# Kernel tuning notes

Hardware: AMD Instinct MI355X
Metric: run time of the kernel (lower is better)

The kernel has to match this reference:

```python
import jax, jax.numpy as jnp
import numpy as np
from jax import lax

K = 8            # number of object slots
H = 250          # hidden / fc_size
EPS = 1e-5
DN = ('NCHW', 'OIHW', 'NCHW')


def ln_all(x):
    # F.layer_norm over all non-batch dims, no affine params (torch init: w=1,b=0)
    ax = tuple(range(1, x.ndim))
    m = jnp.mean(x, ax, keepdims=True)
    v = jnp.var(x, ax, keepdims=True)
    return (x - m) * lax.rsqrt(v + EPS)


def ln_last(x):
    # nn.LayerNorm(feat) -> last dim only
    m = jnp.mean(x, -1, keepdims=True)
    v = jnp.var(x, -1, keepdims=True)
    return (x - m) * lax.rsqrt(v + EPS)


def conv(x, w, b):
    # torch Conv2d(k=4, s=2, p=1), NCHW
    y = lax.conv_general_dilated(x, w, (2, 2), [(1, 1), (1, 1)], dimension_numbers=DN)
    return y + b[None, :, None, None]


def up4(x):
    return jnp.repeat(jnp.repeat(x, 4, axis=2), 4, axis=3)


def setup_inputs():
    ks = jax.random.split(jax.random.key(0), 20)
    bk = 48 * K
    p = lambda i, shape, s: jax.random.normal(ks[i], shape, jnp.float32) * s
    z = lambda n: jnp.zeros((n,), jnp.float32)
    return dict(
        x=p(0, (bk, 4096), 1.0),
        state=p(1, (bk, H), 1.0),
        # encoder convs (OIHW) + fc
        c1w=p(2, (16, 1, 4, 4), 0.25), c1b=z(16),
        c2w=p(3, (32, 16, 4, 4), 0.06), c2b=z(32),
        c3w=p(4, (64, 32, 4, 4), 0.04), c3b=z(64),
        efc_w=p(5, (4096, 512), 0.016), efc_b=z(512),
        # R_NEM (weights stored as [in, out])
        renc_w=p(6, (H, H), 0.06), renc_b=z(H),
        core_w=p(7, (2 * H, H), 0.045), core_b=z(H),
        ctx_w=p(8, (H, H), 0.06), ctx_b=z(H),
        att1_w=p(9, (H, 100), 0.06), att1_b=z(100),
        att2_w=p(10, (100, 1), 0.1), att2_b=z(1),
        out_w=p(11, (2 * H + 512, H), 0.03), out_b=z(H),
        # decoder fcs + convs
        dfc1_w=p(12, (H, 512), 0.06), dfc1_b=z(512),
        dfc2_w=p(13, (512, 4096), 0.045), dfc2_b=z(4096),
        d1w=p(14, (32, 64, 4, 4), 0.03), d1b=z(32),
        d2w=p(15, (16, 32, 4, 4), 0.045), d2b=z(16),
        d3w=p(16, (1, 16, 4, 4), 0.06), d3b=z(1),
    )


def reference(x, state, c1w, c1b, c2w, c2b, c3w, c3b, efc_w, efc_b,
              renc_w, renc_b, core_w, core_b, ctx_w, ctx_b,
              att1_w, att1_b, att2_w, att2_b, out_w, out_b,
              dfc1_w, dfc1_b, dfc2_w, dfc2_b, d1w, d1b, d2w, d2b, d3w, d3b):
    bk = x.shape[0]
    b = bk // K

    # ---------------- EncoderLayer ----------------
    def inwrap(h, w, bias):  # InputWrapper conv branch: NHWC -> permute(0,3,2,1) -> conv -> back
        y = conv(jnp.transpose(h, (0, 3, 2, 1)), w, bias)
        return jax.nn.elu(ln_all(jnp.transpose(y, (0, 3, 2, 1))))

    h = x.reshape(bk, 64, 64, 1)
    h = inwrap(h, c1w, c1b)                 # (bk,32,32,16)
    h = inwrap(h, c2w, c2b)                 # (bk,16,16,32)
    h = inwrap(h, c3w, c3b)                 # (bk,8,8,64)
    h = h.reshape(bk, -1)                   # (bk,4096)
    h = jax.nn.elu(ln_last(h @ efc_w + efc_b))   # (bk,512)

    # ---------------- R_NEM (RecurrentLayer) ----------------
    s1 = jax.nn.relu(ln_last(state @ renc_w + renc_b))   # (bk,H)
    s1r = s1.reshape(b, K, H)
    idx = np.array([[j for j in range(K) if j != i] for i in range(K)])  # (K,K-1)
    cs = s1r[:, idx, :]                                    # context: (b,K,K-1,H)
    fs = jnp.broadcast_to(s1r[:, :, None, :], cs.shape)    # focus copies
    pair = jnp.concatenate([fs, cs], axis=-1)              # (b,K,K-1,2H)
    core = jax.nn.relu(ln_last(pair @ core_w + core_b))    # (b,K,K-1,H)
    ctx = jax.nn.relu(ln_last(core @ ctx_w + ctx_b))       # (b,K,K-1,H)
    att = jax.nn.sigmoid(jnp.tanh(ln_last(core @ att1_w + att1_b)) @ att2_w + att2_b)  # (b,K,K-1,1)
    effect = jnp.sum(ctx * att, axis=2).reshape(bk, H)     # attention-weighted sum over K-1
    total = jnp.concatenate([s1, effect, h], axis=1)       # (bk, 2H+512)
    new_state = total @ out_w + out_b                      # (bk,H)
    xr = jax.nn.sigmoid(ln_last(new_state))
    state_out = jax.nn.sigmoid(new_state)

    # ---------------- DecoderLayer ----------------
    d = jax.nn.relu(ln_last(xr @ dfc1_w + dfc1_b))         # (bk,512)
    d = jax.nn.relu(ln_last(d @ dfc2_w + dfc2_b))          # (bk,4096)
    d = d.reshape(bk, 8, 8, 64)

    def outwrap(t, w, bias):
        y = conv(up4(jnp.transpose(t, (0, 3, 2, 1))), w, bias)
        return jnp.transpose(y, (0, 3, 2, 1))

    d = jax.nn.relu(ln_all(outwrap(d, d1w, d1b)))          # (bk,16,16,32)
    d = jax.nn.relu(ln_all(outwrap(d, d2w, d2b)))          # (bk,32,32,16)
    d = jax.nn.sigmoid(outwrap(d, d3w, d3b))               # (bk,64,64,1), no LN
    x_out = d.reshape(bk, -1)                              # (bk,4096)
    return x_out, state_out
```

## Files before the change

### kernel.cpp

```cpp
#include <hip/hip_runtime.h>
#include <hip/hip_bf16.h>
#include <math.h>

typedef __attribute__((ext_vector_type(8))) short bf16x8;
typedef __attribute__((ext_vector_type(4))) float f32x4;

__device__ __forceinline__ float eluf(float v){ return v > 0.f ? v : expm1f(v); }
__device__ __forceinline__ float sigf(float v){ return 1.f/(1.f+expf(-v)); }
__device__ __forceinline__ unsigned short f2bf(float f){
  unsigned u = __float_as_uint(f);
  u += 0x7FFFu + ((u >> 16) & 1u);
  return (unsigned short)(u >> 16);
}
__device__ __forceinline__ float bf2f(short s){
  return __uint_as_float(((unsigned)(unsigned short)s) << 16);
}

__device__ __forceinline__ void block_reduce2(float& a, float& b, float* sbuf){
  __syncthreads();
  for (int off = 32; off; off >>= 1){
    a += __shfl_down(a, off);
    b += __shfl_down(b, off);
  }
  int lane = threadIdx.x & 63, w = threadIdx.x >> 6;
  if (lane == 0){ sbuf[2*w] = a; sbuf[2*w+1] = b; }
  __syncthreads();
  if (threadIdx.x == 0){
    int nw = blockDim.x >> 6;
    float sa = 0.f, sb = 0.f;
    for (int i = 0; i < nw; i++){ sa += sbuf[2*i]; sb += sbuf[2*i+1]; }
    sbuf[0] = sa; sbuf[1] = sb;
  }
  __syncthreads();
  a = sbuf[0]; b = sbuf[1];
}

__device__ __forceinline__ float fold_sum(const float* __restrict__ w, int O, int I,
                                          int o, int i, int pa, int pb, int da, int db){
  float s = 0.f;
  for (int kh = 0; kh < 4; kh++){
    bool inh = (pb==0) ? (db==0 ? (kh==0) : (kh>=1)) : (db==0 ? (kh<=2) : (kh==3));
    if (!inh) continue;
    for (int kw = 0; kw < 4; kw++){
      bool inw = (pa==0) ? (da==0 ? (kw==0) : (kw>=1)) : (da==0 ? (kw<=2) : (kw==3));
      if (!inw) continue;
      s += w[((o*I + i)*4 + kh)*4 + kw];
    }
  }
  return s;
}
__device__ __forceinline__ void fold_elem(const float* __restrict__ w, float* __restrict__ CW,
                                          int O, int I, int l){
  int o = l % O; int q = l / O;
  int da = q & 1, db = (q>>1)&1, pa = (q>>2)&1, pb = (q>>3)&1, i = q>>4;
  CW[(((pb*2+pa)*4 + db*2+da)*I + i)*O + o] = fold_sum(w, O, I, o, i, pa, pb, da, db);
}
__device__ __forceinline__ void cvtc2_elem(const float* __restrict__ w, short* __restrict__ D, int l){
  int i = l & 15, t = (l>>4) & 15, o = l>>8;
  D[l] = (short)f2bf(w[(o*16 + i)*16 + t]);
}
__device__ __forceinline__ void cvtc3_elem(const float* __restrict__ w, short* __restrict__ D, int l){
  int i = l & 31, t = (l>>5) & 15, o = l>>9;
  D[l] = (short)f2bf(w[(o*32 + i)*16 + t]);
}
__device__ __forceinline__ void foldd1_elem(const float* __restrict__ w, short* __restrict__ D, int l){
  int i = l & 63, tap = (l>>6)&3, o = (l>>8)&31, ph = l>>13;
  D[l] = (short)f2bf(fold_sum(w, 32, 64, o, i, ph&1, ph>>1, tap&1, tap>>1));
}
__device__ __forceinline__ void foldd2_elem(const float* __restrict__ w, short* __restrict__ D, int l){
  int i = l & 31, tap = (l>>5)&3, o = (l>>7)&15, ph = l>>11;
  D[l] = (short)f2bf(fold_sum(w, 16, 32, o, i, ph&1, ph>>1, tap&1, tap>>1));
}

__global__ __launch_bounds__(256) void prep_combined(
  const float* __restrict__ efc,  short* __restrict__ Defc,
  const float* __restrict__ dfc2, short* __restrict__ Ddfc2,
  const float* __restrict__ outw, short* __restrict__ Dout,
  const float* __restrict__ corew,short* __restrict__ Dcore,
  const float* __restrict__ dfc1, short* __restrict__ Ddfc1,
  const float* __restrict__ renc, short* __restrict__ Drenc,
  const float* __restrict__ ctx,  short* __restrict__ Dctx,
  const float* __restrict__ att1, short* __restrict__ Datt1,
  const float* __restrict__ d3w, float* __restrict__ CWT3,
  const float* __restrict__ c2w, short* __restrict__ BtC2,
  const float* __restrict__ c3w, short* __restrict__ BtC3,
  const float* __restrict__ d1w, short* __restrict__ BD1,
  const float* __restrict__ d2w, short* __restrict__ BD2,
  const float* __restrict__ state, short* __restrict__ SBF,
  short* __restrict__ TOTb)
{
  int bx = blockIdx.x;
  if (bx >= 1192){
    const int F3=256, P2=F3+8192, P3=P2+32768, P4=P3+32768, P5=P4+8192,
              ST=P5+98304, TOTAL=ST+4608;
    for (int l = (bx-1192)*256 + threadIdx.x; l < TOTAL; l += 256*256){
      if (l < F3)      fold_elem(d3w, CWT3, 1, 16, l);
      else if (l < P2) cvtc2_elem(c2w, BtC2, l - F3);
      else if (l < P3) cvtc3_elem(c3w, BtC3, l - P2);
      else if (l < P4) foldd1_elem(d1w, BD1, l - P3);
      else if (l < P5) foldd2_elem(d2w, BD2, l - P4);
      else if (l < ST){
        int q = l - P5;
        int n = q >> 8, k = q & 255;
        SBF[q] = (k < 250) ? (short)f2bf(state[n*250 + k]) : (short)0;
      } else {
        int q = l - ST;
        int row = q / 12, cc = q % 12;
        int col = cc < 6 ? 250 + cc : 506 + (cc - 6);
        TOTb[row*1024 + col] = 0;
      }
    }
    return;
  }
  const float* W; short* D; int K, N, Kp, base, mode = 0;
  if      (bx < 512) { W=efc;  D=Defc;  K=4096; N=512;  Kp=4096; base=0;    }
  else if (bx < 1024){ W=dfc2; D=Ddfc2; K=512;  N=4096; Kp=512;  base=512;  }
  else if (bx < 1088){ W=outw; D=Dout;  K=1012; N=250;  Kp=1024; base=1024; mode=2; }
  else if (bx < 1120){ W=corew;D=Dcore; K=500;  N=250;  Kp=512;  base=1088; mode=1; }
  else if (bx < 1152){ W=dfc1; D=Ddfc1; K=250;  N=512;  Kp=256;  base=1120; }
  else if (bx < 1168){ W=renc; D=Drenc; K=250;  N=250;  Kp=256;  base=1152; }
  else if (bx < 1184){ W=ctx;  D=Dctx;  K=250;  N=250;  Kp=256;  base=1168; }
  else               { W=att1; D=Datt1; K=250;  N=100;  Kp=256;  base=1184; }
  int t = bx - base;
  int tpr = Kp >> 6;
  int tk = t % tpr, tn = t / tpr;
  __shared__ short tile[64][65];
  int c = threadIdx.x & 63, r4 = threadIdx.x >> 6;
  int n0 = tn*64, k0 = tk*64;
  #pragma unroll 4
  for (int p = 0; p < 16; p++){
    int r = r4*16 + p;
    int k = k0 + r, n = n0 + c;
    int ksrc = k; bool valid;
    if (mode == 0) valid = (k < K);
    else if (mode == 1){ valid = (k < 250) || (k >= 256 && k < 506); ksrc = k < 256 ? k : k - 6; }
    else { valid = (k < 250) || (k >= 256 && k < 506) || (k >= 512);
           ksrc = k < 256 ? k : (k < 512 ? k - 6 : k - 12); }
    float v = (valid && n < N) ? W[(size_t)ksrc*N + n] : 0.f;
    tile[c][r] = (short)f2bf(v);
  }
  __syncthreads();
  #pragma unroll 4
  for (int p = 0; p < 16; p++){
    int nn = r4*16 + p;
    int n = n0 + nn;
    if (n < N) D[(size_t)n*Kp + k0 + c] = tile[nn][c];
  }
}

__global__ __launch_bounds__(256) void gemm_mfma(
    const short* __restrict__ Ab, const short* __restrict__ Bt,
    float* __restrict__ P, int M, int N, int Kp, int Kc)
{
  __shared__ __align__(16) short As[64*32];
  __shared__ __align__(16) short Bs[64*32];
  int tid = threadIdx.x;
  int bm = blockIdx.y*64, bn = blockIdx.x*64;
  int kb = blockIdx.z * Kc;
  int kend = kb + Kc;

  int r = tid >> 2, c = tid & 3;
  const short* Arow = Ab + (size_t)(bm + r)*Kp;
  int gn = bn + r;
  bool bval = gn < N;
  const short* Brow = Bt + (size_t)gn*Kp;

  uint4 hA, hB;
  auto load_regs = [&](int k0){
    hA = *(const uint4*)&Arow[k0 + c*8];
    hB = bval ? *(const uint4*)&Brow[k0 + c*8] : make_uint4(0,0,0,0);
  };
  auto write_lds = [&](){
    *(uint4*)&As[r*32 + c*8] = hA;
    *(uint4*)&Bs[r*32 + c*8] = hB;
  };

  int wave = tid >> 6;
  int ln = tid & 15, quad = (tid >> 4) & 3;
  int wr = (wave >> 1) * 32, wc = (wave & 1) * 32;

  f32x4 zero = {0.f, 0.f, 0.f, 0.f};
  f32x4 acc[2][2] = {{zero, zero}, {zero, zero}};

  load_regs(kb);
  write_lds();
  __syncthreads();
  for (int k0 = kb; k0 < kend; k0 += 32){
    int nxt = k0 + 32;
    if (nxt < kend) load_regs(nxt);
    bf16x8 a0 = *(const bf16x8*)&As[(wr +      ln)*32 + quad*8];
    bf16x8 a1 = *(const bf16x8*)&As[(wr + 16 + ln)*32 + quad*8];
    bf16x8 b0 = *(const bf16x8*)&Bs[(wc +      ln)*32 + quad*8];
    bf16x8 b1 = *(const bf16x8*)&Bs[(wc + 16 + ln)*32 + quad*8];
    acc[0][0] = __builtin_amdgcn_mfma_f32_16x16x32_bf16(a0, b0, acc[0][0], 0, 0, 0);
    acc[0][1] = __builtin_amdgcn_mfma_f32_16x16x32_bf16(a0, b1, acc[0][1], 0, 0, 0);
    acc[1][0] = __builtin_amdgcn_mfma_f32_16x16x32_bf16(a1, b0, acc[1][0], 0, 0, 0);
    acc[1][1] = __builtin_amdgcn_mfma_f32_16x16x32_bf16(a1, b1, acc[1][1], 0, 0, 0);
    __syncthreads();
    if (nxt < kend){ write_lds(); __syncthreads(); }
  }

  float* Pout = P + (size_t)blockIdx.z*M*N;
  #pragma unroll
  for (int t = 0; t < 2; t++)
    #pragma unroll
    for (int u = 0; u < 2; u++)
      #pragma unroll
      for (int j = 0; j < 4; j++){
        int row = bm + wr + t*16 + quad*4 + j;
        int col = bn + wc + u*16 + ln;
        if (col < N) Pout[(size_t)row*N + col] = acc[t][u][j];
      }
}

__global__ __launch_bounds__(256) void gemm_core_mfma(
    const short* __restrict__ Tb, const short* __restrict__ Bt,
    float* __restrict__ P, int M, int N, int Kc)
{
  __shared__ __align__(16) short As[64*32];
  __shared__ __align__(16) short Bs[64*32];
  int tid = threadIdx.x;
  int bm = blockIdx.y*64, bn = blockIdx.x*64;
  int kb = blockIdx.z * Kc;
  int kend = kb + Kc;

  int r = tid >> 2, c = tid & 3;
  int gr = bm + r;
  int jj2 = gr % 7, fi2 = gr / 7;
  int ii = fi2 & 7, j2 = fi2 >> 3;
  int jidx = jj2 < ii ? jj2 : jj2 + 1;
  const short* own = Tb + (size_t)fi2*1024;
  const short* oth = Tb + (size_t)(j2*8 + jidx)*1024;
  int gn = bn + r;
  bool bval = gn < N;
  const short* Brow = Bt + (size_t)gn*512;

  uint4 hA, hB;
  auto load_regs = [&](int k0){
    int kk = k0 + c*8;
    const short* src = (kk & 256) ? oth : own;
    hA = *(const uint4*)&src[kk & 255];
    hB = bval ? *(const uint4*)&Brow[kk] : make_uint4(0,0,0,0);
  };
  auto write_lds = [&](){
    *(uint4*)&As[r*32 + c*8] = hA;
    *(uint4*)&Bs[r*32 + c*8] = hB;
  };

  int wave = tid >> 6;
  int ln = tid & 15, quad = (tid >> 4) & 3;
  int wr = (wave >> 1) * 32, wc = (wave & 1) * 32;

  f32x4 zero = {0.f, 0.f, 0.f, 0.f};
  f32x4 acc[2][2] = {{zero, zero}, {zero, zero}};

  load_regs(kb);
  write_lds();
  __syncthreads();
  for (int k0 = kb; k0 < kend; k0 += 32){
    int nxt = k0 + 32;
    if (nxt < kend) load_regs(nxt);
    bf16x8 a0 = *(const bf16x8*)&As[(wr +      ln)*32 + quad*8];
    bf16x8 a1 = *(const bf16x8*)&As[(wr + 16 + ln)*32 + quad*8];
    bf16x8 b0 = *(const bf16x8*)&Bs[(wc +      ln)*32 + quad*8];
    bf16x8 b1 = *(const bf16x8*)&Bs[(wc + 16 + ln)*32 + quad*8];
    acc[0][0] = __builtin_amdgcn_mfma_f32_16x16x32_bf16(a0, b0, acc[0][0], 0, 0, 0);
    acc[0][1] = __builtin_amdgcn_mfma_f32_16x16x32_bf16(a0, b1, acc[0][1], 0, 0, 0);
    acc[1][0] = __builtin_amdgcn_mfma_f32_16x16x32_bf16(a1, b0, acc[1][0], 0, 0, 0);
    acc[1][1] = __builtin_amdgcn_mfma_f32_16x16x32_bf16(a1, b1, acc[1][1], 0, 0, 0);
    __syncthreads();
    if (nxt < kend){ write_lds(); __syncthreads(); }
  }

  float* Pout = P + (size_t)blockIdx.z*M*N;
  #pragma unroll
  for (int t = 0; t < 2; t++)
    #pragma unroll
    for (int u = 0; u < 2; u++)
      #pragma unroll
      for (int j = 0; j < 4; j++){
        int row = bm + wr + t*16 + quad*4 + j;
        int col = bn + wc + u*16 + ln;
        if (col < N) Pout[(size_t)row*N + col] = acc[t][u][j];
      }
}

__global__ __launch_bounds__(256) void reduce_ln(
    const float* __restrict__ Pp, const float* __restrict__ bias,
    void* __restrict__ outp, int M, int N, int KS, int os, int act, int obf)
{
  __shared__ float rowbuf[4096];
  __shared__ float sbuf[16];
  int row = blockIdx.x;
  size_t MN = (size_t)M*N;
  float s = 0.f, s2 = 0.f;
  for (int c = threadIdx.x; c < N; c += 256){
    float v = bias[c];
    for (int ks = 0; ks < KS; ks++) v += Pp[ks*MN + (size_t)row*N + c];
    rowbuf[c] = v; s += v; s2 += v*v;
  }
  block_reduce2(s, s2, sbuf);
  float m = s / N;
  float r = rsqrtf(s2/N - m*m + 1e-5f);
  for (int c = threadIdx.x; c < N; c += 256){
    float v = (rowbuf[c]-m)*r;
    if (act == 1) v = fmaxf(v, 0.f);
    else if (act == 2) v = eluf(v);
    else if (act == 3) v = tanhf(v);
    if (obf) ((short*)outp)[(size_t)row*os + c] = f2bf(v);
    else     ((float*)outp)[(size_t)row*os + c] = v;
  }
}

__global__ __launch_bounds__(256) void reduce_ns(
    const float* __restrict__ Pp, const float* __restrict__ bias,
    short* __restrict__ XRb, float* __restrict__ so, int M, int N, int KS)
{
  __shared__ float rowbuf[256];
  __shared__ float sbuf[16];
  int row = blockIdx.x;
  size_t MN = (size_t)M*N;
  float s = 0.f, s2 = 0.f;
  for (int c = threadIdx.x; c < N; c += 256){
    float v = bias[c];
    for (int ks = 0; ks < KS; ks++) v += Pp[ks*MN + (size_t)row*N + c];
    rowbuf[c] = v; s += v; s2 += v*v;
  }
  block_reduce2(s, s2, sbuf);
  float m = s / N;
  float r = rsqrtf(s2/N - m*m + 1e-5f);
  for (int c = threadIdx.x; c < N; c += 256){
    float v = rowbuf[c];
    XRb[(size_t)row*256 + c] = f2bf(sigf((v-m)*r));
    so[(size_t)row*N + c] = sigf(v);
  }
}

__global__ __launch_bounds__(448) void ctx_att_effect(
    const float* __restrict__ Pc, const float* __restrict__ ctx_b,
    const float* __restrict__ Pa, const float* __restrict__ att1_b,
    const float* __restrict__ w2, const float* __restrict__ b2,
    short* __restrict__ tot)
{
  __shared__ float ctxs[7][250];
  __shared__ float att_s[7];
  int fi = blockIdx.x, tid = threadIdx.x;
  int jj = tid >> 6, lane = tid & 63;
  const size_t MN = (size_t)2688*250, MN2 = (size_t)2688*100;
  int row = fi*7 + jj;
  float vv[4];
  float s = 0.f, s2 = 0.f;
  #pragma unroll
  for (int t = 0; t < 4; t++){
    int c = lane + t*64;
    float v = 0.f;
    if (c < 250) v = ctx_b[c] + Pc[(size_t)row*250 + c] + Pc[MN + (size_t)row*250 + c];
    vv[t] = v; s += v; s2 += v*v;
  }
  #pragma unroll
  for (int off = 32; off; off >>= 1){ s += __shfl_down(s, off); s2 += __shfl_down(s2, off); }
  s = __shfl(s, 0); s2 = __shfl(s2, 0);
  float m = s*(1.f/250.f);
  float r = rsqrtf(s2*(1.f/250.f) - m*m + 1e-5f);
  #pragma unroll
  for (int t = 0; t < 4; t++){
    int c = lane + t*64;
    if (c < 250) ctxs[jj][c] = fmaxf((vv[t]-m)*r, 0.f);
  }
  float va[2];
  s = 0.f; s2 = 0.f;
  #pragma unroll
  for (int t = 0; t < 2; t++){
    int c = lane + t*64;
    float v = 0.f;
    if (c < 100){
      v = att1_b[c];
      #pragma unroll
      for (int ks = 0; ks < 4; ks++) v += Pa[ks*MN2 + (size_t)row*100 + c];
    }
    va[t] = v; s += v; s2 += v*v;
  }
  #pragma unroll
  for (int off = 32; off; off >>= 1){ s += __shfl_down(s, off); s2 += __shfl_down(s2, off); }
  s = __shfl(s, 0); s2 = __shfl(s2, 0);
  m = s*0.01f;
  r = rsqrtf(s2*0.01f - m*m + 1e-5f);
  float d = 0.f;
  #pragma unroll
  for (int t = 0; t < 2; t++){
    int c = lane + t*64;
    if (c < 100) d += tanhf((va[t]-m)*r)*w2[c];
  }
  #pragma unroll
  for (int off = 32; off; off >>= 1) d += __shfl_down(d, off);
  if (lane == 0) att_s[jj] = sigf(d + b2[0]);
  __syncthreads();
  for (int h = tid; h < 250; h += 448){
    float sum = 0.f;
    #pragma unroll
    for (int q = 0; q < 7; q++) sum += ctxs[q][h]*att_s[q];
    tot[(size_t)fi*1024 + 256 + h] = f2bf(sum);
  }
}

__global__ __launch_bounds__(256) void enc_conv1_ig(
    const float* __restrict__ x, const float* __restrict__ w, const float* __restrict__ bias,
    short* __restrict__ outp)
{
  __shared__ __align__(16) float in_t[66*68];
  __shared__ short rawb[16384];
  __shared__ float sbuf[16];
  int n = blockIdx.x, tid = threadIdx.x;
  for (int l = tid; l < 66*68; l += 256) in_t[l] = 0.f;
  __syncthreads();
  const float* xin = x + (size_t)n*4096;
  for (int l4 = tid; l4 < 1024; l4 += 256){
    float4 v = *(const float4*)&xin[l4*4];
    int aa = (l4*4) >> 6, bb = (l4*4) & 63;
    float* dst = &in_t[(aa+1)*68 + bb + 1];
    dst[0]=v.x; dst[1]=v.y; dst[2]=v.z; dst[3]=v.w;
  }
  int o = tid & 15;
  float wr[16];
  #pragma unroll
  for (int t = 0; t < 16; t++) wr[t] = w[o*16 + t];
  float bv = bias[o];
  __syncthreads();
  float s = 0.f, s2 = 0.f;
  for (int r = 0; r < 64; r++){
    int idx = tid + (r<<8);
    int bq = (idx>>4)&31, aq = idx>>9;
    int a0 = 2*aq, b0 = 2*bq;
    float acc = bv;
    #pragma unroll
    for (int kw = 0; kw < 4; kw++){
      const float* row = &in_t[(a0+kw)*68 + b0];
      float2 p0 = *(const float2*)&row[0];
      float2 p1 = *(const float2*)&row[2];
      acc += p0.x*wr[0*4+kw] + p0.y*wr[1*4+kw] + p1.x*wr[2*4+kw] + p1.y*wr[3*4+kw];
    }
    rawb[idx] = f2bf(acc);
    s += acc; s2 += acc*acc;
  }
  block_reduce2(s, s2, sbuf);
  float m = s*(1.f/16384.f);
  float rs = rsqrtf(s2*(1.f/16384.f) - m*m + 1e-5f);
  short* op = outp + (size_t)n*16384;
  for (int l = tid; l < 16384; l += 256){
    float v = bf2f(rawb[l]);
    op[l] = f2bf(eluf((v-m)*rs));
  }
}

__global__ __launch_bounds__(256) void enc_conv2_mfma(
    const short* __restrict__ in, const short* __restrict__ Bt, const float* __restrict__ bias,
    short* __restrict__ outp)
{
  __shared__ __align__(16) short in_t[34*34*16];
  __shared__ float sbuf[16];
  int n = blockIdx.x, tid = threadIdx.x;
  for (int l = tid; l < 34*34*16/4; l += 256) ((unsigned long long*)in_t)[l] = 0ull;
  __syncthreads();
  const short* ip = in + (size_t)n*16384;
  for (int l = tid; l < 4096; l += 256){
    int i4 = l & 3, bb = (l>>2) & 31, aa = l>>7;
    *(uint2*)&in_t[((aa+1)*34 + (bb+1))*16 + i4*4] = *(const uint2*)&ip[aa*512 + bb*16 + i4*4];
  }
  int wave = tid>>6, ln = tid&15, quad = (tid>>4)&3;
  bf16x8 bfr[2][8];
  #pragma unroll
  for (int nt = 0; nt < 2; nt++){
    const short* Brow = Bt + (nt*16 + ln)*256;
    #pragma unroll
    for (int ks = 0; ks < 8; ks++)
      bfr[nt][ks] = *(const bf16x8*)&Brow[ks*32 + quad*8];
  }
  __syncthreads();
  f32x4 z = {0.f,0.f,0.f,0.f};
  f32x4 acc[2][4] = {{z,z,z,z},{z,z,z,z}};
  int tapq = quad>>1, io = (quad&1)*8;
  #pragma unroll
  for (int ks = 0; ks < 8; ks++){
    int t = 2*ks + tapq;
    int kh = t>>2, kw = t&3;
    #pragma unroll
    for (int mt = 0; mt < 4; mt++){
      int p = (wave*4 + mt)*16 + ln;
      int oa = p>>4, ob = p&15;
      bf16x8 a = *(const bf16x8*)&in_t[((2*oa+kw)*34 + (2*ob+kh))*16 + io];
      acc[0][mt] = __builtin_amdgcn_mfma_f32_16x16x32_bf16(a, bfr[0][ks], acc[0][mt],0,0,0);
      acc[1][mt] = __builtin_amdgcn_mfma_f32_16x16x32_bf16(a, bfr[1][ks], acc[1][mt],0,0,0);
    }
  }
  float s = 0.f, s2 = 0.f;
  #pragma unroll
  for (int nt = 0; nt < 2; nt++){
    float bz = bias[nt*16 + ln];
    #pragma unroll
    for (int mt = 0; mt < 4; mt++)
      #pragma unroll
      for (int j = 0; j < 4; j++){
        float v = acc[nt][mt][j] + bz;
        acc[nt][mt][j] = v; s += v; s2 += v*v;
      }
  }
  block_reduce2(s, s2, sbuf);
  float m = s*(1.f/8192.f);
  float rs = rsqrtf(s2*(1.f/8192.f) - m*m + 1e-5f);
  short* op = outp + (size_t)n*8192;
  #pragma unroll
  for (int nt = 0; nt < 2; nt++){
    int o = nt*16 + ln;
    #pragma unroll
    for (int mt = 0; mt < 4; mt++)
      #pragma unroll
      for (int j = 0; j < 4; j++){
        int p = (wave*4 + mt)*16 + quad*4 + j;
        int oa = p>>4, ob = p&15;
        op[oa*512 + ob*32 + o] = f2bf(eluf((acc[nt][mt][j]-m)*rs));
      }
  }
}

__global__ __launch_bounds__(256) void enc_conv3_mfma(
    const short* __restrict__ in, const short* __restrict__ Bt, const float* __restrict__ bias,
    short* __restrict__ outp)
{
  __shared__ __align__(16) short in_t[18*18*32];
  __shared__ float sbuf[16];
  int n = blockIdx.x, tid = threadIdx.x;
  for (int l = tid; l < 18*18*32/4; l += 256) ((unsigned long long*)in_t)[l] = 0ull;
  __syncthreads();
  const short* ip = in + (size_t)n*8192;
  for (int l = tid; l < 2048; l += 256){
    int i4 = l & 7, bb = (l>>3)&15, aa = l>>7;
    *(uint2*)&in_t[((aa+1)*18 + (bb+1))*32 + i4*4] = *(const uint2*)&ip[aa*512 + bb*32 + i4*4];
  }
  int wave = tid>>6, ln = tid&15, quad = (tid>>4)&3;
  int o = wave*16 + ln;
  bf16x8 bfr[16];
  {
    const short* Brow = Bt + o*512;
    #pragma unroll
    for (int ks = 0; ks < 16; ks++)
      bfr[ks] = *(const bf16x8*)&Brow[ks*32 + quad*8];
  }
  __syncthreads();
  f32x4 z = {0.f,0.f,0.f,0.f};
  f32x4 acc[4] = {z,z,z,z};
  #pragma unroll
  for (int ks = 0; ks < 16; ks++){
    int kh = ks>>2, kw = ks&3;
    #pragma unroll
    for (int mt = 0; mt < 4; mt++){
      int p = mt*16 + ln;
      int oa = p>>3, ob = p&7;
      bf16x8 a = *(const bf16x8*)&in_t[((2*oa+kw)*18 + (2*ob+kh))*32 + quad*8];
      acc[mt] = __builtin_amdgcn_mfma_f32_16x16x32_bf16(a, bfr[ks], acc[mt],0,0,0);
    }
  }
  float s = 0.f, s2 = 0.f;
  float bz = bias[o];
  #pragma unroll
  for (int mt = 0; mt < 4; mt++)
    #pragma unroll
    for (int j = 0; j < 4; j++){
      float v = acc[mt][j] + bz;
      acc[mt][j] = v; s += v; s2 += v*v;
    }
  block_reduce2(s, s2, sbuf);
  float m = s*(1.f/4096.f);
  float rs = rsqrtf(s2*(1.f/4096.f) - m*m + 1e-5f);
  short* op = outp + (size_t)n*4096;
  #pragma unroll
  for (int mt = 0; mt < 4; mt++)
    #pragma unroll
    for (int j = 0; j < 4; j++){
      int p = mt*16 + quad*4 + j;
      int oa = p>>3, ob = p&7;
      op[oa*512 + ob*64 + o] = f2bf(eluf((acc[mt][j]-m)*rs));
    }
}

__global__ __launch_bounds__(256) void dec_conv1_mfma(
    const short* __restrict__ in, const short* __restrict__ Bd, const float* __restrict__ bias,
    short* __restrict__ outp)
{
  __shared__ __align__(16) short in_t[10*10*64];
  __shared__ float sbuf[16];
  int n = blockIdx.x, tid = threadIdx.x;
  for (int l = tid; l < 10*10*64/4; l += 256) ((unsigned long long*)in_t)[l] = 0ull;
  __syncthreads();
  const short* ip = in + (size_t)n*4096;
  for (int l = tid; l < 1024; l += 256){
    int i4 = l & 15, sb = (l>>4)&7, sa = l>>7;
    *(uint2*)&in_t[((sa+1)*10 + (sb+1))*64 + i4*4] = *(const uint2*)&ip[sa*512 + sb*64 + i4*4];
  }
  int wave = tid>>6, ln = tid&15, quad = (tid>>4)&3;
  int pa = wave & 1, pb = wave >> 1;
  bf16x8 bfr[2][8];
  #pragma unroll
  for (int nt = 0; nt < 2; nt++){
    const short* Brow = Bd + (wave*32 + nt*16 + ln)*256;
    #pragma unroll
    for (int ks = 0; ks < 8; ks++)
      bfr[nt][ks] = *(const bf16x8*)&Brow[ks*32 + quad*8];
  }
  __syncthreads();
  f32x4 z = {0.f,0.f,0.f,0.f};
  f32x4 acc[2][4] = {{z,z,z,z},{z,z,z,z}};
  #pragma unroll
  for (int ks = 0; ks < 8; ks++){
    int tap = ks>>1, ibase = (ks&1)*32 + quad*8;
    int da = tap & 1, db = tap >> 1;
    #pragma unroll
    for (int mt = 0; mt < 4; mt++){
      int p = mt*16 + ln;
      int ta = p>>3, tb = p&7;
      bf16x8 a = *(const bf16x8*)&in_t[((ta+da+pa)*10 + (tb+db+pb))*64 + ibase];
      acc[0][mt] = __builtin_amdgcn_mfma_f32_16x16x32_bf16(a, bfr[0][ks], acc[0][mt],0,0,0);
      acc[1][mt] = __builtin_amdgcn_mfma_f32_16x16x32_bf16(a, bfr[1][ks], acc[1][mt],0,0,0);
    }
  }
  float s = 0.f, s2 = 0.f;
  #pragma unroll
  for (int nt = 0; nt < 2; nt++){
    float bz = bias[nt*16 + ln];
    #pragma unroll
    for (int mt = 0; mt < 4; mt++)
      #pragma unroll
      for (int j = 0; j < 4; j++){
        float v = acc[nt][mt][j] + bz;
        acc[nt][mt][j] = v; s += v; s2 += v*v;
      }
  }
  block_reduce2(s, s2, sbuf);
  float m = s*(1.f/8192.f);
  float rs = rsqrtf(s2*(1.f/8192.f) - m*m + 1e-5f);
  short* op = outp + (size_t)n*8192;
  #pragma unroll
  for (int nt = 0; nt < 2; nt++){
    int o = nt*16 + ln;
    #pragma unroll
    for (int mt = 0; mt < 4; mt++)
      #pragma unroll
      for (int j = 0; j < 4; j++){
        int p = mt*16 + quad*4 + j;
        int ta = p>>3, tb = p&7;
        op[(2*ta+pa)*512 + (2*tb+pb)*32 + o] = f2bf(fmaxf((acc[nt][mt][j]-m)*rs, 0.f));
      }
  }
}

__global__ __launch_bounds__(256) void dec_conv2_mfma(
    const short* __restrict__ in, const short* __restrict__ Bd, const float* __restrict__ bias,
    short* __restrict__ outp)
{
  __shared__ __align__(16) short in_t[18*18*32];
  __shared__ float sbuf[16];
  int n = blockIdx.x, tid = threadIdx.x;
  for (int l = tid; l < 18*18*32/4; l += 256) ((unsigned long long*)in_t)[l] = 0ull;
  __syncthreads();
  const short* ip = in + (size_t)n*8192;
  for (int l = tid; l < 2048; l += 256){
    int i4 = l & 7, sb = (l>>3)&15, sa = l>>7;
    *(uint2*)&in_t[((sa+1)*18 + (sb+1))*32 + i4*4] = *(const uint2*)&ip[sa*512 + sb*32 + i4*4];
  }
  int wave = tid>>6, ln = tid&15, quad = (tid>>4)&3;
  int pa = wave & 1, pb = wave >> 1;
  bf16x8 bfr[4];
  {
    const short* Brow = Bd + (wave*16 + ln)*128;
    #pragma unroll
    for (int ks = 0; ks < 4; ks++)
      bfr[ks] = *(const bf16x8*)&Brow[ks*32 + quad*8];
  }
  __syncthreads();
  f32x4 z = {0.f,0.f,0.f,0.f};
  f32x4 acc[16] = {z,z,z,z,z,z,z,z,z,z,z,z,z,z,z,z};
  #pragma unroll
  for (int ks = 0; ks < 4; ks++){
    int da = ks & 1, db = ks >> 1;
    #pragma unroll
    for (int mt = 0; mt < 16; mt++){
      int p = mt*16 + ln;
      int ta = p>>4, tb = p&15;
      bf16x8 a = *(const bf16x8*)&in_t[((ta+da+pa)*18 + (tb+db+pb))*32 + quad*8];
      acc[mt] = __builtin_amdgcn_mfma_f32_16x16x32_bf16(a, bfr[ks], acc[mt],0,0,0);
    }
  }
  float s = 0.f, s2 = 0.f;
  float bz = bias[ln];
  #pragma unroll
  for (int mt = 0; mt < 16; mt++)
    #pragma unroll
    for (int j = 0; j < 4; j++){
      float v = acc[mt][j] + bz;
      acc[mt][j] = v; s += v; s2 += v*v;
    }
  block_reduce2(s, s2, sbuf);
  float m = s*(1.f/16384.f);
  float rs = rsqrtf(s2*(1.f/16384.f) - m*m + 1e-5f);
  short* op = outp + (size_t)n*16384;
  #pragma unroll
  for (int mt = 0; mt < 16; mt++)
    #pragma unroll
    for (int j = 0; j < 4; j++){
      int p = mt*16 + quad*4 + j;
      int ta = p>>4, tb = p&15;
      op[(2*ta+pa)*512 + (2*tb+pb)*16 + ln] = f2bf(fmaxf((acc[mt][j]-m)*rs, 0.f));
    }
}

__global__ __launch_bounds__(256) void dec_conv3_ig(
    const short* __restrict__ in, const float* __restrict__ CWT, const float* __restrict__ bias,
    float* __restrict__ outp)
{
  __shared__ __align__(16) float in_t[9792];
  __shared__ __align__(16) float wl[256];
  int bx = blockIdx.x;
  int n = bx >> 1, b0 = (bx & 1) * 32, tb0 = b0 >> 1;
  int tid = threadIdx.x;
  const short* ip = in + (size_t)n*16384;
  for (int l = tid; l < 9792; l += 256){
    int i = l & 15, sb = (l >> 4) % 18, sap = l / 288;
    int sa = sap - 1, sbg = tb0 - 1 + sb;
    float v = 0.f;
    if ((unsigned)sa < 32u && (unsigned)sbg < 32u)
      v = bf2f(ip[sa*512 + sbg*16 + i]);
    in_t[(sap*18 + sb)*16 + i] = v;
  }
  for (int l = tid; l < 256; l += 256) wl[l] = CWT[l];
  __syncthreads();
  float bv = bias[0];
  int bl = tid & 31, ath = tid >> 5;
  int b = b0 + bl;
  int tb = b >> 1, pb = b & 1;
  float* op = outp + (size_t)n*4096;
  #pragma unroll
  for (int j = 0; j < 8; j++){
    int a = ath*8 + j;
    int ta = a >> 1, pa = a & 1;
    float4 s4 = make_float4(0.f,0.f,0.f,0.f);
    #pragma unroll
    for (int db = 0; db < 2; db++){
      int sb = tb + db + (pb ? 0 : -1);
      int sbl = sb - (tb0 - 1);
      #pragma unroll
      for (int da = 0; da < 2; da++){
        int sa = ta + da + (pa ? 0 : -1);
        int sap = sa + 1;
        const float4* A4 = (const float4*)&in_t[(sap*18 + sbl)*16];
        const float4* B4 = (const float4*)&wl[((pb*2+pa)*4 + db*2+da)*16];
        #pragma unroll
        for (int q = 0; q < 4; q++){
          float4 av = A4[q], bw = B4[q];
          s4.x += av.x*bw.x; s4.y += av.y*bw.y;
          s4.z += av.z*bw.z; s4.w += av.w*bw.w;
        }
      }
    }
    op[a*64 + b] = sigf(bv + s4.x + s4.y + s4.z + s4.w);
  }
}

extern "C" void kernel_launch(void* const* d_in, const int* in_sizes, int n_in,
                              void* d_out, int out_size, void* d_ws, size_t ws_size,
                              hipStream_t stream) {
  const float* x      = (const float*)d_in[0];
  const float* state  = (const float*)d_in[1];
  const float* c1w    = (const float*)d_in[2];
  const float* c1b    = (const float*)d_in[3];
  const float* c2w    = (const float*)d_in[4];
  const float* c2b    = (const float*)d_in[5];
  const float* c3w    = (const float*)d_in[6];
  const float* c3b    = (const float*)d_in[7];
  const float* efc_w  = (const float*)d_in[8];
  const float* efc_b  = (const float*)d_in[9];
  const float* renc_w = (const float*)d_in[10];
  const float* renc_b = (const float*)d_in[11];
  const float* core_w = (const float*)d_in[12];
  const float* core_b = (const float*)d_in[13];
  const float* ctx_w  = (const float*)d_in[14];
  const float* ctx_b  = (const float*)d_in[15];
  const float* att1_w = (const float*)d_in[16];
  const float* att1_b = (const float*)d_in[17];
  const float* att2_w = (const float*)d_in[18];
  const float* att2_b = (const float*)d_in[19];
  const float* out_w  = (const float*)d_in[20];
  const float* out_b  = (const float*)d_in[21];
  const float* dfc1_w = (const float*)d_in[22];
  const float* dfc1_b = (const float*)d_in[23];
  const float* dfc2_w = (const float*)d_in[24];
  const float* dfc2_b = (const float*)d_in[25];
  const float* d1w    = (const float*)d_in[26];
  const float* d1b    = (const float*)d_in[27];
  const float* d2w    = (const float*)d_in[28];
  const float* d2b    = (const float*)d_in[29];
  const float* d3w    = (const float*)d_in[30];
  const float* d3b    = (const float*)d_in[31];

  float* wsf = (float*)d_ws;
  size_t o = 0;
  float* PB   = wsf + o; o += (size_t)1600*1024;
  float* PB2  = wsf + o; o += (size_t)2688*100*4;
  float* CWT3 = wsf + o; o += 256;
  short* E1b  = (short*)(wsf + o); o += (size_t)384*16384/2;
  short* E2b  = (short*)(wsf + o); o += (size_t)384*8192/2;
  short* E3b  = (short*)(wsf + o); o += (size_t)384*4096/2;
  short* TOTb = (short*)(wsf + o); o += (size_t)384*1024/2;
  short* C1b  = (short*)(wsf + o); o += (size_t)2688*256/2;
  short* XRb  = (short*)(wsf + o); o += (size_t)384*256/2;
  short* G1b  = (short*)(wsf + o); o += (size_t)384*512/2;
  short* SBF  = (short*)(wsf + o); o += (size_t)384*256/2;
  short* BtC2 = (short*)(wsf + o); o += 8192/2;
  short* BtC3 = (short*)(wsf + o); o += 32768/2;
  short* BD1  = (short*)(wsf + o); o += 32768/2;
  short* BD2  = (short*)(wsf + o); o += 8192/2;
  short* BT_efc  = (short*)(wsf + o); o += 2097152/2;
  short* BT_renc = (short*)(wsf + o); o += 64000/2;
  short* BT_core = (short*)(wsf + o); o += 128000/2;
  short* BT_ctx  = (short*)(wsf + o); o += 64000/2;
  short* BT_att1 = (short*)(wsf + o); o += 25600/2;
  short* BT_out  = (short*)(wsf + o); o += 256000/2;
  short* BT_dfc1 = (short*)(wsf + o); o += 131072/2;
  short* BT_dfc2 = (short*)(wsf + o); o += 2097152/2;
  short* D1b = E2b;
  short* D2b = E1b;
  short* G2b = E3b;

  float* xout = (float*)d_out;
  float* sout = xout + (size_t)384*4096;

  prep_combined<<<1448, 256, 0, stream>>>(
      efc_w, BT_efc, dfc2_w, BT_dfc2, out_w, BT_out, core_w, BT_core,
      dfc1_w, BT_dfc1, renc_w, BT_renc, ctx_w, BT_ctx, att1_w, BT_att1,
      d3w, CWT3, c2w, BtC2, c3w, BtC3, d1w, BD1, d2w, BD2, state, SBF, TOTb);

  enc_conv1_ig<<<384, 256, 0, stream>>>(x, c1w, c1b, E1b);
  enc_conv2_mfma<<<384, 256, 0, stream>>>(E1b, BtC2, c2b, E2b);
  enc_conv3_mfma<<<384, 256, 0, stream>>>(E2b, BtC3, c3b, E3b);
  gemm_mfma<<<dim3(8,6,8), 256, 0, stream>>>(E3b, BT_efc, PB, 384, 512, 4096, 512);
  reduce_ln<<<384, 256, 0, stream>>>(PB, efc_b, TOTb+512, 384, 512, 8, 1024, 2, 1);

  gemm_mfma<<<dim3(4,6,8), 256, 0, stream>>>(SBF, BT_renc, PB, 384, 250, 256, 32);
  reduce_ln<<<384, 256, 0, stream>>>(PB, renc_b, TOTb, 384, 250, 8, 1024, 1, 1);
  gemm_core_mfma<<<dim3(4,42,2), 256, 0, stream>>>(TOTb, BT_core, PB, 2688, 250, 256);
  reduce_ln<<<2688, 256, 0, stream>>>(PB, core_b, C1b, 2688, 250, 2, 256, 1, 1);
  gemm_mfma<<<dim3(4,42,2), 256, 0, stream>>>(C1b, BT_ctx, PB, 2688, 250, 256, 128);
  gemm_mfma<<<dim3(2,42,4), 256, 0, stream>>>(C1b, BT_att1, PB2, 2688, 100, 256, 64);
  ctx_att_effect<<<384, 448, 0, stream>>>(PB, ctx_b, PB2, att1_b, att2_w, att2_b, TOTb);

  gemm_mfma<<<dim3(4,6,8), 256, 0, stream>>>(TOTb, BT_out, PB, 384, 250, 1024, 128);
  reduce_ns<<<384, 256, 0, stream>>>(PB, out_b, XRb, sout, 384, 250, 8);

  gemm_mfma<<<dim3(8,6,4), 256, 0, stream>>>(XRb, BT_dfc1, PB, 384, 512, 256, 64);
  reduce_ln<<<384, 256, 0, stream>>>(PB, dfc1_b, G1b, 384, 512, 4, 512, 1, 1);
  gemm_mfma<<<dim3(64,6,1), 256, 0, stream>>>(G1b, BT_dfc2, PB, 384, 4096, 512, 512);
  reduce_ln<<<384, 256, 0, stream>>>(PB, dfc2_b, G2b, 384, 4096, 1, 4096, 1, 1);

  dec_conv1_mfma<<<384, 256, 0, stream>>>(G2b, BD1, d1b, D1b);
  dec_conv2_mfma<<<384, 256, 0, stream>>>(D1b, BD2, d2b, D2b);
  dec_conv3_ig<<<768, 256, 0, stream>>>(D2b, CWT3, d3b, xout);

  (void)in_sizes; (void)n_in; (void)out_size; (void)ws_size;
}
```

Baseline: 334.7 us.

## Fuse encoder conv2+conv3 and decoder conv1+conv2 through shared memory

Merges two pairs of consecutive per-sample conv kernels into single kernels. The intermediate activation is written into padded shared memory instead of global memory, and the next conv reads it from there. This removes two kernel launches and a global write and read of the intermediate tensor per pair. In exchange, one block runs both stages with more registers live (weights for the second stage are loaded early), which may reduce occupancy. The smem buffer is reused, so it has to be re-zeroed, with an extra barrier between the stages.

```diff
diff --git a/kernel.cpp b/kernel.cpp
--- a/kernel.cpp
+++ b/kernel.cpp
@@ -452,25 +452,25 @@
   }
 }
 
-__global__ __launch_bounds__(256) void enc_conv2_mfma(
-    const short* __restrict__ in, const short* __restrict__ Bt, const float* __restrict__ bias,
-    short* __restrict__ outp)
-{
-  __shared__ __align__(16) short in_t[34*34*16];
+__global__ __launch_bounds__(256) void enc_conv23_mfma(
+    const short* __restrict__ in, const short* __restrict__ Bt2, const float* __restrict__ bias2,
+    const short* __restrict__ Bt3, const float* __restrict__ bias3, short* __restrict__ outp)
+{
+  __shared__ __align__(16) short smem[34*34*16];
   __shared__ float sbuf[16];
   int n = blockIdx.x, tid = threadIdx.x;
-  for (int l = tid; l < 34*34*16/4; l += 256) ((unsigned long long*)in_t)[l] = 0ull;
+  for (int l = tid; l < 34*34*16/4; l += 256) ((unsigned long long*)smem)[l] = 0ull;
   __syncthreads();
   const short* ip = in + (size_t)n*16384;
   for (int l = tid; l < 4096; l += 256){
     int i4 = l & 3, bb = (l>>2) & 31, aa = l>>7;
-    *(uint2*)&in_t[((aa+1)*34 + (bb+1))*16 + i4*4] = *(const uint2*)&ip[aa*512 + bb*16 + i4*4];
+    *(uint2*)&smem[((aa+1)*34 + (bb+1))*16 + i4*4] = *(const uint2*)&ip[aa*512 + bb*16 + i4*4];
   }
   int wave = tid>>6, ln = tid&15, quad = (tid>>4)&3;
   bf16x8 bfr[2][8];
   #pragma unroll
   for (int nt = 0; nt < 2; nt++){
-    const short* Brow = Bt + (nt*16 + ln)*256;
+    const short* Brow = Bt2 + (nt*16 + ln)*256;
     #pragma unroll
     for (int ks = 0; ks < 8; ks++)
       bfr[nt][ks] = *(const bf16x8*)&Brow[ks*32 + quad*8];
@@ -487,7 +487,7 @@
     for (int mt = 0; mt < 4; mt++){
       int p = (wave*4 + mt)*16 + ln;
       int oa = p>>4, ob = p&15;
-      bf16x8 a = *(const bf16x8*)&in_t[((2*oa+kw)*34 + (2*ob+kh))*16 + io];
+      bf16x8 a = *(const bf16x8*)&smem[((2*oa+kw)*34 + (2*ob+kh))*16 + io];
       acc[0][mt] = __builtin_amdgcn_mfma_f32_16x16x32_bf16(a, bfr[0][ks], acc[0][mt],0,0,0);
       acc[1][mt] = __builtin_amdgcn_mfma_f32_16x16x32_bf16(a, bfr[1][ks], acc[1][mt],0,0,0);
     }
@@ -495,7 +495,7 @@
   float s = 0.f, s2 = 0.f;
   #pragma unroll
   for (int nt = 0; nt < 2; nt++){
-    float bz = bias[nt*16 + ln];
+    float bz = bias2[nt*16 + ln];
     #pragma unroll
     for (int mt = 0; mt < 4; mt++)
       #pragma unroll
@@ -505,9 +505,18 @@
       }
   }
   block_reduce2(s, s2, sbuf);
-  float m = s*(1.f/8192.f);
-  float rs = rsqrtf(s2*(1.f/8192.f) - m*m + 1e-5f);
-  short* op = outp + (size_t)n*8192;
+  float m2 = s*(1.f/8192.f);
+  float rs2 = rsqrtf(s2*(1.f/8192.f) - m2*m2 + 1e-5f);
+  int o3 = wave*16 + ln;
+  bf16x8 bfr3[16];
+  {
+    const short* Brow = Bt3 + o3*512;
+    #pragma unroll
+    for (int ks = 0; ks < 16; ks++)
+      bfr3[ks] = *(const bf16x8*)&Brow[ks*32 + quad*8];
+  }
+  for (int l = tid; l < 2592; l += 256) ((unsigned long long*)smem)[l] = 0ull;
+  __syncthreads();
   #pragma unroll
   for (int nt = 0; nt < 2; nt++){
     int o = nt*16 + ln;
@@ -517,37 +526,11 @@
       for (int j = 0; j < 4; j++){
         int p = (wave*4 + mt)*16 + quad*4 + j;
         int oa = p>>4, ob = p&15;
-        op[oa*512 + ob*32 + o] = f2bf(eluf((acc[nt][mt][j]-m)*rs));
+        smem[((oa+1)*18 + (ob+1))*32 + o] = f2bf(eluf((acc[nt][mt][j]-m2)*rs2));
       }
   }
-}
-
-__global__ __launch_bounds__(256) void enc_conv3_mfma(
-    const short* __restrict__ in, const short* __restrict__ Bt, const float* __restrict__ bias,
-    short* __restrict__ outp)
-{
-  __shared__ __align__(16) short in_t[18*18*32];
-  __shared__ float sbuf[16];
-  int n = blockIdx.x, tid = threadIdx.x;
-  for (int l = tid; l < 18*18*32/4; l += 256) ((unsigned long long*)in_t)[l] = 0ull;
-  __syncthreads();
-  const short* ip = in + (size_t)n*8192;
-  for (int l = tid; l < 2048; l += 256){
-    int i4 = l & 7, bb = (l>>3)&15, aa = l>>7;
-    *(uint2*)&in_t[((aa+1)*18 + (bb+1))*32 + i4*4] = *(const uint2*)&ip[aa*512 + bb*32 + i4*4];
-  }
-  int wave = tid>>6, ln = tid&15, quad = (tid>>4)&3;
-  int o = wave*16 + ln;
-  bf16x8 bfr[16];
-  {
-    const short* Brow = Bt + o*512;
-    #pragma unroll
-    for (int ks = 0; ks < 16; ks++)
-      bfr[ks] = *(const bf16x8*)&Brow[ks*32 + quad*8];
-  }
-  __syncthreads();
-  f32x4 z = {0.f,0.f,0.f,0.f};
-  f32x4 acc[4] = {z,z,z,z};
+  __syncthreads();
+  f32x4 acc3[4] = {z,z,z,z};
   #pragma unroll
   for (int ks = 0; ks < 16; ks++){
     int kh = ks>>2, kw = ks&3;
@@ -555,22 +538,22 @@
     for (int mt = 0; mt < 4; mt++){
       int p = mt*16 + ln;
       int oa = p>>3, ob = p&7;
-      bf16x8 a = *(const bf16x8*)&in_t[((2*oa+kw)*18 + (2*ob+kh))*32 + quad*8];
-      acc[mt] = __builtin_amdgcn_mfma_f32_16x16x32_bf16(a, bfr[ks], acc[mt],0,0,0);
-    }
-  }
-  float s = 0.f, s2 = 0.f;
-  float bz = bias[o];
+      bf16x8 a = *(const bf16x8*)&smem[((2*oa+kw)*18 + (2*ob+kh))*32 + quad*8];
+      acc3[mt] = __builtin_amdgcn_mfma_f32_16x16x32_bf16(a, bfr3[ks], acc3[mt],0,0,0);
+    }
+  }
+  s = 0.f; s2 = 0.f;
+  float bz3 = bias3[o3];
   #pragma unroll
   for (int mt = 0; mt < 4; mt++)
     #pragma unroll
     for (int j = 0; j < 4; j++){
-      float v = acc[mt][j] + bz;
-      acc[mt][j] = v; s += v; s2 += v*v;
+      float v = acc3[mt][j] + bz3;
+      acc3[mt][j] = v; s += v; s2 += v*v;
     }
   block_reduce2(s, s2, sbuf);
-  float m = s*(1.f/4096.f);
-  float rs = rsqrtf(s2*(1.f/4096.f) - m*m + 1e-5f);
+  float m3 = s*(1.f/4096.f);
+  float rs3 = rsqrtf(s2*(1.f/4096.f) - m3*m3 + 1e-5f);
   short* op = outp + (size_t)n*4096;
   #pragma unroll
   for (int mt = 0; mt < 4; mt++)
@@ -578,33 +561,33 @@
     for (int j = 0; j < 4; j++){
       int p = mt*16 + quad*4 + j;
       int oa = p>>3, ob = p&7;
-      op[oa*512 + ob*64 + o] = f2bf(eluf((acc[mt][j]-m)*rs));
-    }
-}
-
-__global__ __launch_bounds__(256) void dec_conv1_mfma(
-    const short* __restrict__ in, const short* __restrict__ Bd, const float* __restrict__ bias,
-    short* __restrict__ outp)
-{
-  __shared__ __align__(16) short in_t[10*10*64];
+      op[oa*512 + ob*64 + o3] = f2bf(eluf((acc3[mt][j]-m3)*rs3));
+    }
+}
+
+__global__ __launch_bounds__(256) void dec_conv12_mfma(
+    const short* __restrict__ in, const short* __restrict__ Bd1, const float* __restrict__ bias1,
+    const short* __restrict__ Bd2, const float* __restrict__ bias2, short* __restrict__ outp)
+{
+  __shared__ __align__(16) short smem[18*18*32];
   __shared__ float sbuf[16];
   int n = blockIdx.x, tid = threadIdx.x;
-  for (int l = tid; l < 10*10*64/4; l += 256) ((unsigned long long*)in_t)[l] = 0ull;
+  for (int l = tid; l < 1600; l += 256) ((unsigned long long*)smem)[l] = 0ull;
   __syncthreads();
   const short* ip = in + (size_t)n*4096;
   for (int l = tid; l < 1024; l += 256){
     int i4 = l & 15, sb = (l>>4)&7, sa = l>>7;
-    *(uint2*)&in_t[((sa+1)*10 + (sb+1))*64 + i4*4] = *(const uint2*)&ip[sa*512 + sb*64 + i4*4];
+    *(uint2*)&smem[((sa+1)*10 + (sb+1))*64 + i4*4] = *(const uint2*)&ip[sa*512 + sb*64 + i4*4];
   }
   int wave = tid>>6, ln = tid&15, quad = (tid>>4)&3;
   int pa = wave & 1, pb = wave >> 1;
-  bf16x8 bfr[2][8];
+  bf16x8 bfr1[2][8];
   #pragma unroll
   for (int nt = 0; nt < 2; nt++){
-    const short* Brow = Bd + (wave*32 + nt*16 + ln)*256;
+    const short* Brow = Bd1 + (wave*32 + nt*16 + ln)*256;
     #pragma unroll
     for (int ks = 0; ks < 8; ks++)
-      bfr[nt][ks] = *(const bf16x8*)&Brow[ks*32 + quad*8];
+      bfr1[nt][ks] = *(const bf16x8*)&Brow[ks*32 + quad*8];
   }
   __syncthreads();
   f32x4 z = {0.f,0.f,0.f,0.f};
@@ -617,15 +600,15 @@
     for (int mt = 0; mt < 4; mt++){
       int p = mt*16 + ln;
       int ta = p>>3, tb = p&7;
-      bf16x8 a = *(const bf16x8*)&in_t[((ta+da+pa)*10 + (tb+db+pb))*64 + ibase];
-      acc[0][mt] = __builtin_amdgcn_mfma_f32_16x16x32_bf16(a, bfr[0][ks], acc[0][mt],0,0,0);
-      acc[1][mt] = __builtin_amdgcn_mfma_f32_16x16x32_bf16(a, bfr[1][ks], acc[1][mt],0,0,0);
+      bf16x8 a = *(const bf16x8*)&smem[((ta+da+pa)*10 + (tb+db+pb))*64 + ibase];
+      acc[0][mt] = __builtin_amdgcn_mfma_f32_16x16x32_bf16(a, bfr1[0][ks], acc[0][mt],0,0,0);
+      acc[1][mt] = __builtin_amdgcn_mfma_f32_16x16x32_bf16(a, bfr1[1][ks], acc[1][mt],0,0,0);
     }
   }
   float s = 0.f, s2 = 0.f;
   #pragma unroll
   for (int nt = 0; nt < 2; nt++){
-    float bz = bias[nt*16 + ln];
+    float bz = bias1[nt*16 + ln];
     #pragma unroll
     for (int mt = 0; mt < 4; mt++)
       #pragma unroll
@@ -635,9 +618,17 @@
       }
   }
   block_reduce2(s, s2, sbuf);
-  float m = s*(1.f/8192.f);
-  float rs = rsqrtf(s2*(1.f/8192.f) - m*m + 1e-5f);
-  short* op = outp + (size_t)n*8192;
+  float m1 = s*(1.f/8192.f);
+  float rs1 = rsqrtf(s2*(1.f/8192.f) - m1*m1 + 1e-5f);
+  bf16x8 bfr2[4];
+  {
+    const short* Brow = Bd2 + (wave*16 + ln)*128;
+    #pragma unroll
+    for (int ks = 0; ks < 4; ks++)
+      bfr2[ks] = *(const bf16x8*)&Brow[ks*32 + quad*8];
+  }
+  for (int l = tid; l < 2592; l += 256) ((unsigned long long*)smem)[l] = 0ull;
+  __syncthreads();
   #pragma unroll
   for (int nt = 0; nt < 2; nt++){
     int o = nt*16 + ln;
@@ -647,37 +638,12 @@
       for (int j = 0; j < 4; j++){
         int p = mt*16 + quad*4 + j;
         int ta = p>>3, tb = p&7;
-        op[(2*ta+pa)*512 + (2*tb+pb)*32 + o] = f2bf(fmaxf((acc[nt][mt][j]-m)*rs, 0.f));
+        int sa = 2*ta + pa, sb = 2*tb + pb;
+        smem[((sa+1)*18 + (sb+1))*32 + o] = f2bf(fmaxf((acc[nt][mt][j]-m1)*rs1, 0.f));
       }
   }
-}
-
-__global__ __launch_bounds__(256) void dec_conv2_mfma(
-    const short* __restrict__ in, const short* __restrict__ Bd, const float* __restrict__ bias,
-    short* __restrict__ outp)
-{
-  __shared__ __align__(16) short in_t[18*18*32];
-  __shared__ float sbuf[16];
-  int n = blockIdx.x, tid = threadIdx.x;
-  for (int l = tid; l < 18*18*32/4; l += 256) ((unsigned long long*)in_t)[l] = 0ull;
-  __syncthreads();
-  const short* ip = in + (size_t)n*8192;
-  for (int l = tid; l < 2048; l += 256){
-    int i4 = l & 7, sb = (l>>3)&15, sa = l>>7;
-    *(uint2*)&in_t[((sa+1)*18 + (sb+1))*32 + i4*4] = *(const uint2*)&ip[sa*512 + sb*32 + i4*4];
-  }
-  int wave = tid>>6, ln = tid&15, quad = (tid>>4)&3;
-  int pa = wave & 1, pb = wave >> 1;
-  bf16x8 bfr[4];
-  {
-    const short* Brow = Bd + (wave*16 + ln)*128;
-    #pragma unroll
-    for (int ks = 0; ks < 4; ks++)
-      bfr[ks] = *(const bf16x8*)&Brow[ks*32 + quad*8];
-  }
-  __syncthreads();
-  f32x4 z = {0.f,0.f,0.f,0.f};
-  f32x4 acc[16] = {z,z,z,z,z,z,z,z,z,z,z,z,z,z,z,z};
+  __syncthreads();
+  f32x4 acc2[16] = {z,z,z,z,z,z,z,z,z,z,z,z,z,z,z,z};
   #pragma unroll
   for (int ks = 0; ks < 4; ks++){
     int da = ks & 1, db = ks >> 1;
@@ -685,18 +651,18 @@
     for (int mt = 0; mt < 16; mt++){
       int p = mt*16 + ln;
       int ta = p>>4, tb = p&15;
-      bf16x8 a = *(const bf16x8*)&in_t[((ta+da+pa)*18 + (tb+db+pb))*32 + quad*8];
-      acc[mt] = __builtin_amdgcn_mfma_f32_16x16x32_bf16(a, bfr[ks], acc[mt],0,0,0);
-    }
-  }
-  float s = 0.f, s2 = 0.f;
-  float bz = bias[ln];
+      bf16x8 a = *(const bf16x8*)&smem[((ta+da+pa)*18 + (tb+db+pb))*32 + quad*8];
+      acc2[mt] = __builtin_amdgcn_mfma_f32_16x16x32_bf16(a, bfr2[ks], acc2[mt],0,0,0);
+    }
+  }
+  s = 0.f; s2 = 0.f;
+  float bz2 = bias2[ln];
   #pragma unroll
   for (int mt = 0; mt < 16; mt++)
     #pragma unroll
     for (int j = 0; j < 4; j++){
-      float v = acc[mt][j] + bz;
-      acc[mt][j] = v; s += v; s2 += v*v;
+      float v = acc2[mt][j] + bz2;
+      acc2[mt][j] = v; s += v; s2 += v*v;
     }
   block_reduce2(s, s2, sbuf);
   float m = s*(1.f/16384.f);
@@ -708,7 +674,7 @@
     for (int j = 0; j < 4; j++){
       int p = mt*16 + quad*4 + j;
       int ta = p>>4, tb = p&15;
-      op[(2*ta+pa)*512 + (2*tb+pb)*16 + ln] = f2bf(fmaxf((acc[mt][j]-m)*rs, 0.f));
+      op[(2*ta+pa)*512 + (2*tb+pb)*16 + ln] = f2bf(fmaxf((acc2[mt][j]-m)*rs, 0.f));
     }
 }
 
@@ -825,9 +791,9 @@
   short* BT_out  = (short*)(wsf + o); o += 256000/2;
   short* BT_dfc1 = (short*)(wsf + o); o += 131072/2;
   short* BT_dfc2 = (short*)(wsf + o); o += 2097152/2;
-  short* D1b = E2b;
   short* D2b = E1b;
   short* G2b = E3b;
+  (void)E2b;
 
   float* xout = (float*)d_out;
   float* sout = xout + (size_t)384*4096;
@@ -838,8 +804,7 @@
       d3w, CWT3, c2w, BtC2, c3w, BtC3, d1w, BD1, d2w, BD2, state, SBF, TOTb);
 
   enc_conv1_ig<<<384, 256, 0, stream>>>(x, c1w, c1b, E1b);
-  enc_conv2_mfma<<<384, 256, 0, stream>>>(E1b, BtC2, c2b, E2b);
-  enc_conv3_mfma<<<384, 256, 0, stream>>>(E2b, BtC3, c3b, E3b);
+  enc_conv23_mfma<<<384, 256, 0, stream>>>(E1b, BtC2, c2b, BtC3, c3b, E3b);
   gemm_mfma<<<dim3(8,6,8), 256, 0, stream>>>(E3b, BT_efc, PB, 384, 512, 4096, 512);
   reduce_ln<<<384, 256, 0, stream>>>(PB, efc_b, TOTb+512, 384, 512, 8, 1024, 2, 1);
 
@@ -859,8 +824,7 @@
   gemm_mfma<<<dim3(64,6,1), 256, 0, stream>>>(G1b, BT_dfc2, PB, 384, 4096, 512, 512);
   reduce_ln<<<384, 256, 0, stream>>>(PB, dfc2_b, G2b, 384, 4096, 1, 4096, 1, 1);
 
-  dec_conv1_mfma<<<384, 256, 0, stream>>>(G2b, BD1, d1b, D1b);
-  dec_conv2_mfma<<<384, 256, 0, stream>>>(D1b, BD2, d2b, D2b);
+  dec_conv12_mfma<<<384, 256, 0, stream>>>(G2b, BD1, d1b, BD2, d2b, D2b);
   dec_conv3_ig<<<768, 256, 0, stream>>>(D2b, CWT3, d3b, xout);
 
   (void)in_sizes; (void)n_in; (void)out_size; (void)ws_size;
```

Result: faster. 322.5 us (-3.6%).
